# Kernel optimization log

Hardware: AMD Instinct MI355X
Metric: run time of the kernel (lower is better)

## Reference

```python
import jax, jax.numpy as jnp
import numpy as np
import math

D_MODEL = 1024
NHEAD = 16
HEAD_DIM = D_MODEL // NHEAD
ROPE_BASE = 10000.0


def _rope(x):
    # x: [B, H, S, Dh]; rotate per the RoPE class (half-split variant)
    d = x.shape[-1]
    half = d // 2
    seq_len = x.shape[2]
    theta = 1.0 / (ROPE_BASE ** (jnp.arange(0, d, 2, dtype=jnp.float32) / d))  # [d/2]
    ang = jnp.arange(seq_len, dtype=jnp.float32)[:, None] * theta[None, :]      # [S, d/2]
    ang2 = jnp.concatenate([ang, ang], axis=-1)                                 # [S, d]
    cos_ = jnp.cos(ang2)[None, None, :, :]
    sin_ = jnp.sin(ang2)[None, None, :, :]
    neg_half = jnp.concatenate([-x[..., half:], x[..., :half]], axis=-1)
    return x * cos_ + neg_half * sin_


def setup_inputs() -> dict:
    key = jax.random.key(0)
    ks = jax.random.split(key, 10)
    B, S, D = 4, 2048, D_MODEL
    scale = 1.0 / math.sqrt(D)
    x = jax.random.normal(ks[0], (B, S, D), dtype=jnp.float32)
    Wq = jax.random.normal(ks[1], (D, D), dtype=jnp.float32) * scale
    bq = jnp.zeros((D,), dtype=jnp.float32)
    Wk = jax.random.normal(ks[2], (D, D), dtype=jnp.float32) * scale
    bk = jnp.zeros((D,), dtype=jnp.float32)
    Wv = jax.random.normal(ks[3], (D, D), dtype=jnp.float32) * scale
    bv = jnp.zeros((D,), dtype=jnp.float32)
    Wo = jax.random.normal(ks[4], (D, D), dtype=jnp.float32) * scale
    bo = jnp.zeros((D,), dtype=jnp.float32)
    # causal mask: mask==1 means masked (upper triangle)
    mask = jnp.triu(jnp.ones((S, S), dtype=jnp.int32), k=1)[None, None, :, :]
    return {"x": x, "Wq": Wq, "bq": bq, "Wk": Wk, "bk": bk,
            "Wv": Wv, "bv": bv, "Wo": Wo, "bo": bo, "mask": mask}


def reference(x, Wq, bq, Wk, bk, Wv, bv, Wo, bo, mask):
    B, S, D = x.shape
    H, Dh = NHEAD, HEAD_DIM

    def proj(W, b):
        y = jnp.einsum('bsd,ed->bse', x, W) + b  # torch Linear: x @ W.T + b
        return y.reshape(B, S, H, Dh).transpose(0, 2, 1, 3)  # [B,H,S,Dh]

    q = _rope(proj(Wq, bq))
    k = _rope(proj(Wk, bk))
    v = proj(Wv, bv)

    a = jnp.einsum('bhqd,bhkd->bhqk', q, k) / math.sqrt(Dh)  # [B,H,S,S]
    a = jnp.where(mask == 1, jnp.float32(-1e9), a)
    a = jax.nn.softmax(a, axis=-1)
    out = jnp.einsum('bhqk,bhkd->bhqd', a, v)                 # [B,H,S,Dh]
    out = out.transpose(0, 2, 1, 3).reshape(B, S, D)
    return jnp.einsum('bsd,ed->bse', out, Wo) + bo
```

## Files before the change

### kernel.cpp

```cpp
#include <hip/hip_runtime.h>
#include <stdint.h>

typedef unsigned short u16;
typedef __bf16 bf16x8 __attribute__((ext_vector_type(8)));
typedef __bf16 bf16x2 __attribute__((ext_vector_type(2)));
typedef float f32x4 __attribute__((ext_vector_type(4)));
typedef float f32x16 __attribute__((ext_vector_type(16)));

#define SEQ    2048
#define NHEAD  16
#define DH     64
#define DMODEL 1024
#define NBH    64

__device__ __forceinline__ u16 cvt1(float f){
  union { __bf16 h; u16 u; } c; c.h = (__bf16)f; return c.u;
}
__device__ __forceinline__ uint32_t cvt2(float a, float b){
  union { bf16x2 v; uint32_t u; } c; c.v = bf16x2{(__bf16)a, (__bf16)b}; return c.u;
}
__device__ __forceinline__ int swz(int row){ return (((row&7)^((row>>3)&7))<<4); }

#if __has_builtin(__builtin_amdgcn_exp2f)
__device__ __forceinline__ float EXP2(float x){ return __builtin_amdgcn_exp2f(x); }
#else
__device__ __forceinline__ float EXP2(float x){ return exp2f(x); }
#endif
__device__ __forceinline__ float max3f(float a, float b, float c){
  float r; asm("v_max3_f32 %0, %1, %2, %3" : "=v"(r) : "v"(a), "v"(b), "v"(c));
  return r;
}

typedef const __attribute__((address_space(1))) uint32_t* gas_t;
typedef __attribute__((address_space(3))) uint32_t* las_t;
__device__ __forceinline__ void async16(const void* g, void* l){
  __builtin_amdgcn_global_load_lds((gas_t)g, (las_t)l, 16, 0, 0);
}

__device__ __forceinline__ void vstore8(char* dst, uint2 a0, uint2 a1,
                                        uint2 b0, uint2 b1, int dc, int vpos){
  uint32_t pk[8];
  pk[0] = __builtin_amdgcn_perm(b0.x, a0.x, 0x05040100u);
  pk[1] = __builtin_amdgcn_perm(b0.x, a0.x, 0x07060302u);
  pk[2] = __builtin_amdgcn_perm(b0.y, a0.y, 0x05040100u);
  pk[3] = __builtin_amdgcn_perm(b0.y, a0.y, 0x07060302u);
  pk[4] = __builtin_amdgcn_perm(b1.x, a1.x, 0x05040100u);
  pk[5] = __builtin_amdgcn_perm(b1.x, a1.x, 0x07060302u);
  pk[6] = __builtin_amdgcn_perm(b1.y, a1.y, 0x05040100u);
  pk[7] = __builtin_amdgcn_perm(b1.y, a1.y, 0x07060302u);
#pragma unroll
  for (int e=0;e<8;e++){
    const int row = dc*8 + e;
    *(uint32_t*)(dst + ((row*128 + vpos*2) ^ swz(row))) = pk[e];
  }
}

__global__ void prep(const float* __restrict__ x,  const float* __restrict__ Wq,
                     const float* __restrict__ Wk, const float* __restrict__ Wv,
                     const float* __restrict__ Wo,
                     u16* __restrict__ xb, u16* __restrict__ wqkv,
                     u16* __restrict__ wob, float* __restrict__ tab)
{
  const int bid = blockIdx.x, tid = threadIdx.x;
  if (bid < 6144){
    const float* src; u16* dst; int lb;
    if      (bid < 4096){ src = x;  dst = xb;              lb = bid; }
    else if (bid < 4608){ src = Wq; dst = wqkv;            lb = bid-4096; }
    else if (bid < 5120){ src = Wk; dst = wqkv + 1048576;  lb = bid-4608; }
    else if (bid < 5632){ src = Wv; dst = wqkv + 2097152;  lb = bid-5120; }
    else                { src = Wo; dst = wob;             lb = bid-5632; }
    const size_t off = (size_t)lb*2048 + tid*8;
    float4 a = *(const float4*)(src+off);
    float4 b = *(const float4*)(src+off+4);
    bf16x8 o = { (__bf16)a.x,(__bf16)a.y,(__bf16)a.z,(__bf16)a.w,
                 (__bf16)b.x,(__bf16)b.y,(__bf16)b.z,(__bf16)b.w };
    *(bf16x8*)(dst+off) = o;
  } else {
    const int t = (bid-6144)*256 + tid;
    const int s = t >> 5, j = t & 31;
    double freq = exp(-(double)(2*j)/64.0*log(10000.0));
    double ang = (double)s*freq;
    tab[s*64 + 2*j]     = (float)cos(ang);
    tab[s*64 + 2*j + 1] = (float)sin(ang);
  }
}

template<int MODE>
__global__ __launch_bounds__(256, 2)
void gemm_bt(const u16* __restrict__ A, const u16* __restrict__ W,
             const float* __restrict__ b0, const float* __restrict__ b1,
             const float* __restrict__ b2, float* __restrict__ fout,
             u16* __restrict__ dq, u16* __restrict__ dk, u16* __restrict__ dv,
             const float* __restrict__ tab)
{
  __shared__ u16 Ab[128*32];
  __shared__ u16 Bb[128*32];
  const int tid = threadIdx.x;
  const int lane = tid & 63;
  const int w = tid >> 6, wr = w >> 1, wc = w & 1;
  const int m0 = blockIdx.y * 128;
  const int n0 = blockIdx.x * 128;
  const int c0 = lane & 15, g = lane >> 4;

  f32x4 acc[4][4] = {};

  const int sr = tid >> 2;
  const int sc16 = tid & 3;
  const int stoff = sr*64 + sc16*16;
  const int gsw = (sc16*16) ^ ((sr & 3) << 4);
  const char* ga = (const char*)A + (size_t)(m0 + sr)*DMODEL*2 + gsw;
  const char* gb = (const char*)W + (size_t)(n0 + sr)*DMODEL*2 + gsw;

  for (int k0 = 0; k0 < DMODEL; k0 += 32) {
    __syncthreads();
    async16(ga + 2*k0,              (char*)Ab + stoff);
    async16(ga + 2*k0 + 128*DMODEL, (char*)Ab + stoff + 4096);
    async16(gb + 2*k0,              (char*)Bb + stoff);
    async16(gb + 2*k0 + 128*DMODEL, (char*)Bb + stoff + 4096);
    __syncthreads();
    bf16x8 afr[4], bfr[4];
#pragma unroll
    for (int i=0;i<4;i++){
      const int row = wr*64 + i*16 + c0;
      afr[i] = *(const bf16x8*)((const char*)Ab + row*64 + ((g*16) ^ ((row&3)<<4)));
    }
#pragma unroll
    for (int j=0;j<4;j++){
      const int row = wc*64 + j*16 + c0;
      bfr[j] = *(const bf16x8*)((const char*)Bb + row*64 + ((g*16) ^ ((row&3)<<4)));
    }
    __builtin_amdgcn_s_setprio(1);
#pragma unroll
    for (int i=0;i<4;i++)
#pragma unroll
      for (int j=0;j<4;j++)
        acc[i][j] = __builtin_amdgcn_mfma_f32_16x16x32_bf16(afr[i], bfr[j], acc[i][j], 0,0,0);
    __builtin_amdgcn_s_setprio(0);
  }

  const int nbase = n0 + wc*64;
  const int t = n0 >> 10;
  const float* bias = (MODE==1) ? b0 : (t==0) ? b0 : (t==1) ? b1 : b2;
  float bv4[4];
#pragma unroll
  for (int j=0;j<4;j++) bv4[j] = bias[(nbase & 1023) + j*16 + c0];

  if (MODE == 0) {
    u16* dst = (t==0) ? dq : (t==1) ? dk : dv;
    const float qs = (t==0) ? 0.18033688011f : 1.0f;
    const int h = (nbase >> 6) & (NHEAD-1);
#pragma unroll
    for (int i=0;i<4;i++){
      const int mbase = m0 + wr*64 + i*16 + g*4;
#pragma unroll
      for (int r=0;r<4;r++){
        const int mm = mbase + r;
        const int bb = mm >> 11, s = mm & (SEQ-1);
        const size_t rowbase = (((size_t)(bb*NHEAD + h))*SEQ + s)*DH;
        if (t < 2) {
#pragma unroll
          for (int j2=0;j2<2;j2++){
            const int dh = j2*16 + c0;
            const float xl = acc[i][j2][r]   + bv4[j2];
            const float xh = acc[i][j2+2][r] + bv4[j2+2];
            const float2 cs = *(const float2*)(tab + (size_t)s*64 + dh*2);
            dst[rowbase + dh]      = cvt1((xl*cs.x - xh*cs.y)*qs);
            dst[rowbase + dh + 32] = cvt1((xh*cs.x + xl*cs.y)*qs);
          }
        } else {
#pragma unroll
          for (int j=0;j<4;j++)
            dst[rowbase + j*16 + c0] = cvt1(acc[i][j][r] + bv4[j]);
        }
      }
    }
  } else {
#pragma unroll
    for (int i=0;i<4;i++){
      const int mbase = m0 + wr*64 + i*16 + g*4;
#pragma unroll
      for (int j=0;j<4;j++){
#pragma unroll
        for (int r=0;r<4;r++)
          fout[(size_t)(mbase + r) * DMODEL + nbase + j*16 + c0] = acc[i][j][r] + bv4[j];
      }
    }
  }
}

__global__ __launch_bounds__(256, 2)
void attn_fwd(const u16* __restrict__ Q, const u16* __restrict__ K,
              const u16* __restrict__ V, u16* __restrict__ O)
{
  __shared__ u16 Kb[2][64*64];
  __shared__ u16 Vt[2][64*64];
  const int bh = blockIdx.x;
  const int pair = blockIdx.y;
  const int tid = threadIdx.x, lane = tid & 63, w = tid >> 6;
  const int c31 = lane & 31, hi = lane >> 5;
  const size_t hb = (size_t)bh * SEQ * DH;
  const int b = bh >> 4, h = bh & 15;

  const int boff1 = tid*16;
  const int ksw1  = boff1 ^ swz(boff1 >> 7);
  const int boff2 = boff1 + 4096;
  const int ksw2  = boff2 ^ swz(boff2 >> 7);
  const int rp = tid >> 3, dc = tid & 7;
  const int kv0 = 2*rp;
  const int vpos = (kv0 & 0x33) | ((kv0 & 4) << 1) | ((kv0 & 8) >> 1);

#pragma unroll 1
  for (int half = 0; half < 2; half++){
    const int qt = half ? (15 - pair) : pair;
    const int qrow_base = qt*128 + w*32;
    const int jt_last  = 2*qt + 1;
    const int jt_end_w = 2*qt + (w>>1);
    const int q = qrow_base + c31;

    bf16x8 qf[4];
#pragma unroll
    for (int kc=0;kc<4;kc++)
      qf[kc] = *(const bf16x8*)(Q + hb + (size_t)q*DH + kc*16 + hi*8);

    f32x16 oacc0 = {}, oacc1 = {};
    float mrun = -3.0e38f, lrun = 0.f;

    {
      const char* gk = (const char*)(K + hb);
      async16(gk + ksw1, (char*)Kb[0] + boff1);
      async16(gk + ksw2, (char*)Kb[0] + boff2);
      const u16* gv = V + hb;
      uint2 a0 = *(const uint2*)(gv + (kv0  )*DH + dc*8);
      uint2 a1 = *(const uint2*)(gv + (kv0  )*DH + dc*8 + 4);
      uint2 b0 = *(const uint2*)(gv + (kv0+1)*DH + dc*8);
      uint2 b1 = *(const uint2*)(gv + (kv0+1)*DH + dc*8 + 4);
      vstore8((char*)Vt[0], a0, a1, b0, b1, dc, vpos);
    }
    __syncthreads();

    uint2 pa0, pa1, pb0, pb1;
    for (int jt = 0; jt <= jt_last; jt++){
      const int cur = jt & 1, nxt = cur ^ 1;
      const bool pre = (jt < jt_last);
      if (pre){
        const char* gk = (const char*)(K + hb + (size_t)(jt+1)*64*DH);
        async16(gk + ksw1, (char*)Kb[nxt] + boff1);
        async16(gk + ksw2, (char*)Kb[nxt] + boff2);
        const u16* gv = V + hb + (size_t)(jt+1)*64*DH;
        pa0 = *(const uint2*)(gv + (kv0  )*DH + dc*8);
        pa1 = *(const uint2*)(gv + (kv0  )*DH + dc*8 + 4);
        pb0 = *(const uint2*)(gv + (kv0+1)*DH + dc*8);
        pb1 = *(const uint2*)(gv + (kv0+1)*DH + dc*8 + 4);
      }

      if (jt <= jt_end_w){
        f32x16 sT[2] = {};
#pragma unroll
        for (int kc=0;kc<4;kc++){
          const int col = (kc*16 + hi*8)*2;
          const int r0 = c31, r1 = 32 + c31;
          const bf16x8 kf0 = *(const bf16x8*)((const char*)Kb[cur] + ((r0*128 + col) ^ swz(r0)));
          const bf16x8 kf1 = *(const bf16x8*)((const char*)Kb[cur] + ((r1*128 + col) ^ swz(r1)));
          __builtin_amdgcn_s_setprio(1);
          sT[0] = __builtin_amdgcn_mfma_f32_32x32x16_bf16(kf0, qf[kc], sT[0], 0,0,0);
          sT[1] = __builtin_amdgcn_mfma_f32_32x32x16_bf16(kf1, qf[kc], sT[1], 0,0,0);
          __builtin_amdgcn_s_setprio(0);
        }
        if (jt == jt_end_w){
#pragma unroll
          for (int kvb=0;kvb<2;kvb++)
#pragma unroll
            for (int r=0;r<16;r++){
              const int kv = jt*64 + kvb*32 + (r&3) + 8*(r>>2) + 4*hi;
              sT[kvb][r] = (kv <= q) ? sT[kvb][r] : -3.0e38f;
            }
        }
        float mx0 = -3.0e38f, mx1 = -3.0e38f;
#pragma unroll
        for (int r=0;r<16;r+=2){
          mx0 = max3f(mx0, sT[0][r], sT[0][r+1]);
          mx1 = max3f(mx1, sT[1][r], sT[1][r+1]);
        }
        float mx = fmaxf(mx0, mx1);
        mx = fmaxf(mx, __shfl_xor(mx, 32));
        const bool grow = __any(mx > mrun + 8.0f);
        float corr = 1.0f;
        if (grow){
          const float mnew = fmaxf(mrun, mx);
          corr = EXP2(mrun - mnew);
          mrun = mnew;
        }
        float ls[4] = {0.f, 0.f, 0.f, 0.f};
#pragma unroll
        for (int kvb=0;kvb<2;kvb++)
#pragma unroll
          for (int r=0;r<16;r++){
            const float p = EXP2(sT[kvb][r] - mrun);
            sT[kvb][r] = p;
            ls[r & 3] += p;
          }
        float lsum = (ls[0] + ls[1]) + (ls[2] + ls[3]);
        lsum += __shfl_xor(lsum, 32);
        lrun = lrun*corr + lsum;
        if (grow){
#pragma unroll
          for (int r=0;r<16;r++){ oacc0[r] *= corr; oacc1[r] *= corr; }
        }
#pragma unroll
        for (int kvb=0;kvb<2;kvb++)
#pragma unroll
          for (int s=0;s<2;s++){
            union { bf16x8 v; uint32_t d[4]; } pa;
#pragma unroll
            for (int j=0;j<4;j++)
              pa.d[j] = cvt2(sT[kvb][s*8+2*j], sT[kvb][s*8+2*j+1]);
            const int col = (kvb*32 + s*16 + hi*8)*2;
            const int r0 = c31, r1 = 32 + c31;
            const bf16x8 vf0 = *(const bf16x8*)((const char*)Vt[cur] + ((r0*128 + col) ^ swz(r0)));
            const bf16x8 vf1 = *(const bf16x8*)((const char*)Vt[cur] + ((r1*128 + col) ^ swz(r1)));
            __builtin_amdgcn_s_setprio(1);
            oacc0 = __builtin_amdgcn_mfma_f32_32x32x16_bf16(vf0, pa.v, oacc0, 0,0,0);
            oacc1 = __builtin_amdgcn_mfma_f32_32x32x16_bf16(vf1, pa.v, oacc1, 0,0,0);
            __builtin_amdgcn_s_setprio(0);
          }
      }

      if (pre) vstore8((char*)Vt[nxt], pa0, pa1, pb0, pb1, dc, vpos);
      __syncthreads();
    }

    {
      const float inv = 1.0f / lrun;
      u16* orow = O + ((size_t)b*SEQ + q)*DMODEL + h*DH;
#pragma unroll
      for (int r2=0;r2<8;r2++){
        const int dh0 = 2*(r2&1) + 8*(r2>>1) + 4*hi;
        *(uint32_t*)(orow + dh0)      = cvt2(oacc0[2*r2]*inv, oacc0[2*r2+1]*inv);
        *(uint32_t*)(orow + 32 + dh0) = cvt2(oacc1[2*r2]*inv, oacc1[2*r2+1]*inv);
      }
    }
  }
}

extern "C" void kernel_launch(void* const* d_in, const int* in_sizes, int n_in,
                              void* d_out, int out_size, void* d_ws, size_t ws_size,
                              hipStream_t stream)
{
  const float* x  = (const float*)d_in[0];
  const float* Wq = (const float*)d_in[1];
  const float* bq = (const float*)d_in[2];
  const float* Wk = (const float*)d_in[3];
  const float* bk = (const float*)d_in[4];
  const float* Wv = (const float*)d_in[5];
  const float* bv = (const float*)d_in[6];
  const float* Wo = (const float*)d_in[7];
  const float* bo = (const float*)d_in[8];

  const size_t MB = 1024*1024;
  char* ws = (char*)d_ws;
  u16*  xb   = (u16*)(ws);
  u16*  aw   = (u16*)(ws);
  u16*  vw   = (u16*)(ws + 16*MB);
  u16*  wqkv = (u16*)(ws + 32*MB);
  u16*  wob  = (u16*)(ws + 38*MB);
  float* tab = (float*)(ws + 41*MB);
  u16*  qw = (u16*)d_out;
  u16*  kw = (u16*)d_out + 8*MB;

  prep<<<dim3(6400), dim3(256), 0, stream>>>(x, Wq, Wk, Wv, Wo, xb, wqkv, wob, tab);

  gemm_bt<0><<<dim3(24, 64), dim3(256), 0, stream>>>(xb, wqkv, bq, bk, bv,
                                                     nullptr, qw, kw, vw, tab);

  attn_fwd<<<dim3(64, 8), dim3(256), 0, stream>>>(qw, kw, vw, aw);

  gemm_bt<1><<<dim3(8, 64), dim3(256), 0, stream>>>(aw, wob, bo, nullptr, nullptr,
                                                    (float*)d_out, nullptr, nullptr, nullptr, nullptr);
}
```

Measured before the change: 175.0 us.

## Deepen GEMM K-tile to 64, remap blocks for L2 locality, raise occupancy

The QKV and output GEMMs now stage a 64-wide K slice per iteration in a 128-byte-row LDS layout with an 8-way XOR swizzle, which halves the number of barrier pairs per K sweep. A 1D grid is remapped so that consecutive blocks share N tiles and interleave M tiles, to improve L2 reuse of the weight and activation tiles. Launch bounds are raised to 4 blocks per CU. The doubled LDS footprint and the higher occupancy target may raise register pressure or cause spills.

```diff
diff --git a/kernel.cpp b/kernel.cpp
--- a/kernel.cpp
+++ b/kernel.cpp
@@ -86,55 +86,62 @@
 }
 
 template<int MODE>
-__global__ __launch_bounds__(256, 2)
+__global__ __launch_bounds__(256, 4)
 void gemm_bt(const u16* __restrict__ A, const u16* __restrict__ W,
              const float* __restrict__ b0, const float* __restrict__ b1,
              const float* __restrict__ b2, float* __restrict__ fout,
              u16* __restrict__ dq, u16* __restrict__ dk, u16* __restrict__ dv,
              const float* __restrict__ tab)
 {
-  __shared__ u16 Ab[128*32];
-  __shared__ u16 Bb[128*32];
+  __shared__ u16 Ab[128*64];
+  __shared__ u16 Bb[128*64];
   const int tid = threadIdx.x;
   const int lane = tid & 63;
   const int w = tid >> 6, wr = w >> 1, wc = w & 1;
-  const int m0 = blockIdx.y * 128;
-  const int n0 = blockIdx.x * 128;
+  const int id = blockIdx.x;
+  const int bx = id >> 6;
+  const int by = ((id & 7) << 3) | ((id >> 3) & 7);
+  const int m0 = by * 128;
+  const int n0 = bx * 128;
   const int c0 = lane & 15, g = lane >> 4;
 
   f32x4 acc[4][4] = {};
 
-  const int sr = tid >> 2;
-  const int sc16 = tid & 3;
-  const int stoff = sr*64 + sc16*16;
-  const int gsw = (sc16*16) ^ ((sr & 3) << 4);
-  const char* ga = (const char*)A + (size_t)(m0 + sr)*DMODEL*2 + gsw;
-  const char* gb = (const char*)W + (size_t)(n0 + sr)*DMODEL*2 + gsw;
-
-  for (int k0 = 0; k0 < DMODEL; k0 += 32) {
+  const int srow = tid >> 3;
+  const int gcol = (((tid & 7) ^ (srow & 7)) << 4);
+  const char* ga = (const char*)A + (size_t)(m0 + srow)*2048 + gcol;
+  const char* gb = (const char*)W + (size_t)(n0 + srow)*2048 + gcol;
+  const int ldst = tid*16;
+
+#pragma unroll 1
+  for (int it = 0; it < 16; ++it) {
+    const int kbyte = it*128;
     __syncthreads();
-    async16(ga + 2*k0,              (char*)Ab + stoff);
-    async16(ga + 2*k0 + 128*DMODEL, (char*)Ab + stoff + 4096);
-    async16(gb + 2*k0,              (char*)Bb + stoff);
-    async16(gb + 2*k0 + 128*DMODEL, (char*)Bb + stoff + 4096);
+#pragma unroll
+    for (int k=0;k<4;k++){
+      async16(ga + kbyte + k*32*2048, (char*)Ab + k*4096 + ldst);
+      async16(gb + kbyte + k*32*2048, (char*)Bb + k*4096 + ldst);
+    }
     __syncthreads();
-    bf16x8 afr[4], bfr[4];
-#pragma unroll
-    for (int i=0;i<4;i++){
-      const int row = wr*64 + i*16 + c0;
-      afr[i] = *(const bf16x8*)((const char*)Ab + row*64 + ((g*16) ^ ((row&3)<<4)));
-    }
-#pragma unroll
-    for (int j=0;j<4;j++){
-      const int row = wc*64 + j*16 + c0;
-      bfr[j] = *(const bf16x8*)((const char*)Bb + row*64 + ((g*16) ^ ((row&3)<<4)));
+    bf16x8 afr[2][4], bfr[2][4];
+#pragma unroll
+    for (int kk=0;kk<2;kk++){
+#pragma unroll
+      for (int i=0;i<4;i++){
+        const int ra = wr*64 + i*16 + c0;
+        afr[kk][i] = *(const bf16x8*)((const char*)Ab + ra*128 + ((((kk*4+g) ^ (ra&7))) << 4));
+        const int rb = wc*64 + i*16 + c0;
+        bfr[kk][i] = *(const bf16x8*)((const char*)Bb + rb*128 + ((((kk*4+g) ^ (rb&7))) << 4));
+      }
     }
     __builtin_amdgcn_s_setprio(1);
 #pragma unroll
-    for (int i=0;i<4;i++)
-#pragma unroll
-      for (int j=0;j<4;j++)
-        acc[i][j] = __builtin_amdgcn_mfma_f32_16x16x32_bf16(afr[i], bfr[j], acc[i][j], 0,0,0);
+    for (int kk=0;kk<2;kk++)
+#pragma unroll
+      for (int i=0;i<4;i++)
+#pragma unroll
+        for (int j=0;j<4;j++)
+          acc[i][j] = __builtin_amdgcn_mfma_f32_16x16x32_bf16(afr[kk][i], bfr[kk][j], acc[i][j], 0,0,0);
     __builtin_amdgcn_s_setprio(0);
   }
 
@@ -369,11 +376,11 @@
 
   prep<<<dim3(6400), dim3(256), 0, stream>>>(x, Wq, Wk, Wv, Wo, xb, wqkv, wob, tab);
 
-  gemm_bt<0><<<dim3(24, 64), dim3(256), 0, stream>>>(xb, wqkv, bq, bk, bv,
-                                                     nullptr, qw, kw, vw, tab);
+  gemm_bt<0><<<dim3(1536), dim3(256), 0, stream>>>(xb, wqkv, bq, bk, bv,
+                                                   nullptr, qw, kw, vw, tab);
 
   attn_fwd<<<dim3(64, 8), dim3(256), 0, stream>>>(qw, kw, vw, aw);
 
-  gemm_bt<1><<<dim3(8, 64), dim3(256), 0, stream>>>(aw, wob, bo, nullptr, nullptr,
-                                                    (float*)d_out, nullptr, nullptr, nullptr, nullptr);
-}
+  gemm_bt<1><<<dim3(512), dim3(256), 0, stream>>>(aw, wob, bo, nullptr, nullptr,
+                                                  (float*)d_out, nullptr, nullptr, nullptr, nullptr);
+}
```

Measured after the change: 197.0 us. +12.6%, slower.
